# Kernel optimization log

Measured on AMD Instinct MI355X. Metric: run time of the kernel, lower is better.

## Reference

```python
import jax, jax.numpy as jnp
import numpy as np

N_HEADS = 4
NEG_SLOPE = 0.2  # DGL GATConv default leaky_relu slope


def setup_inputs() -> dict:
    key = jax.random.key(0)
    ks = jax.random.split(key, 12)
    N, E = 50000, 800000
    in_dim, time_dim, out_dim = 128, 128, 128
    d_head = out_dim // N_HEADS
    in_total = in_dim + time_dim
    h = jax.random.normal(ks[0], (N, in_dim), jnp.float32)
    time_tensor = jax.random.uniform(ks[1], (E,), jnp.float32)
    src = jax.random.randint(ks[2], (E,), 0, N, jnp.int32)
    dst = jax.random.randint(ks[3], (E,), 0, N, jnp.int32)
    # TimeEncoding: Linear(1, time_dim) with xavier weight, zero bias
    w_t = jax.random.normal(ks[4], (time_dim, 1), jnp.float32) * (6.0 / (1 + time_dim)) ** 0.5
    b_t = jnp.zeros((time_dim,), jnp.float32)
    # GATConv params
    W_fc = jax.random.normal(ks[5], (N_HEADS * d_head, in_total), jnp.float32) * (2.0 / in_total) ** 0.5
    attn_l = jax.random.normal(ks[6], (N_HEADS, d_head), jnp.float32) * 0.1
    attn_r = jax.random.normal(ks[7], (N_HEADS, d_head), jnp.float32) * 0.1
    W_res = jax.random.normal(ks[8], (N_HEADS * d_head, in_total), jnp.float32) * (2.0 / in_total) ** 0.5
    bias = jnp.zeros((N_HEADS * d_head,), jnp.float32)
    return {"h": h, "time_tensor": time_tensor, "src": src, "dst": dst,
            "num_nodes": N, "w_t": w_t, "b_t": b_t, "W_fc": W_fc,
            "attn_l": attn_l, "attn_r": attn_r, "W_res": W_res, "bias": bias}


def reference(h, time_tensor, src, dst, num_nodes, w_t, b_t, W_fc, attn_l, attn_r, W_res, bias):
    N = num_nodes
    E = src.shape[0]
    # Time encoding: cos(W t + b), per edge -> [E, time_dim]
    time_emb = jnp.cos(time_tensor[:, None] * w_t[:, 0][None, :] + b_t[None, :])
    # Mailbox mean of concat([src h, time_emb]) per dst node.
    # mean(concat) == concat(mean, mean), so sum the two halves separately.
    ones = jnp.ones((E,), h.dtype)
    deg = jax.ops.segment_sum(ones, dst, num_segments=N)  # [N]
    sum_h = jax.ops.segment_sum(h[src], dst, num_segments=N)       # [N, in_dim]
    sum_t = jax.ops.segment_sum(time_emb, dst, num_segments=N)     # [N, time_dim]
    inv_deg = 1.0 / jnp.maximum(deg, 1.0)
    h_time = jnp.concatenate([sum_h, sum_t], axis=1) * inv_deg[:, None]  # [N, in+time]
    # GATConv (eval mode, no dropout)
    d_head = W_fc.shape[0] // N_HEADS
    feat = (h_time @ W_fc.T).reshape(N, N_HEADS, d_head)  # [N,H,D]
    el = jnp.sum(feat * attn_l[None], axis=-1)  # [N,H]
    er = jnp.sum(feat * attn_r[None], axis=-1)  # [N,H]
    e = el[src] + er[dst]                        # [E,H]
    e = jnp.where(e > 0, e, NEG_SLOPE * e)
    # edge softmax over incoming edges of each dst node
    m = jax.ops.segment_max(e, dst, num_segments=N)  # [N,H]
    m = jnp.where(jnp.isfinite(m), m, 0.0)
    ex = jnp.exp(e - m[dst])
    denom = jax.ops.segment_sum(ex, dst, num_segments=N)
    a = ex / jnp.maximum(denom[dst], 1e-9)           # [E,H]
    rst = jax.ops.segment_sum(a[:, :, None] * feat[src], dst, num_segments=N)  # [N,H,D]
    res = (h_time @ W_res.T).reshape(N, N_HEADS, d_head)
    out = rst + res + bias.reshape(1, N_HEADS, d_head)
    out = jax.nn.elu(out)
    return out.reshape(N, -1)  # [N, out_dim]
```

## Files before the change

### kernel.cpp

```cpp
#include <hip/hip_runtime.h>
#include <math.h>

#define NH 4
#define NEG_SLOPE 0.2f
#define BKT_SHIFT 8
#define EPB 4096
#define CBLK 8192
#define TBLK 512
#define INV2PI 0.15915494309189535f
#define LOG2E  1.4426950408889634f

typedef __attribute__((ext_vector_type(8))) short bf16x8;
typedef __attribute__((ext_vector_type(4))) float f32x4;
typedef __attribute__((ext_vector_type(2))) float f32x2;

__device__ __forceinline__ float blo(unsigned u) { return __uint_as_float(u << 16); }
__device__ __forceinline__ float bhi(unsigned u) { return __uint_as_float(u & 0xFFFF0000u); }
__device__ __forceinline__ f32x2 mk2(float a, float b) { f32x2 r; r.x = a; r.y = b; return r; }
__device__ __forceinline__ f32x2 unpk(unsigned u) { return mk2(blo(u), bhi(u)); }
__device__ __forceinline__ unsigned short rne(float f) {
    unsigned u = __float_as_uint(f);
    u += 0x7FFFu + ((u >> 16) & 1u);
    return (unsigned short)(u >> 16);
}
__device__ __forceinline__ unsigned pack2(float a, float b) {
    return (unsigned)rne(a) | ((unsigned)rne(b) << 16);
}

__global__ __launch_bounds__(256) void k_prep(
    const float* __restrict__ h, unsigned* __restrict__ hbu, int n_pairs,
    const float* __restrict__ Wfc, const float* __restrict__ Wres,
    unsigned* __restrict__ wcat,
    const float* __restrict__ w_t, const float* __restrict__ b_t,
    unsigned* __restrict__ tbl,
    const int* __restrict__ dst, int* __restrict__ bkt_cnt, int E, int NB, int EB) {
    __shared__ int cnt[256];
    int tid = threadIdx.x;
    int t = blockIdx.x * blockDim.x + tid;
    if (t < n_pairs) {
        float2 v = ((const float2*)h)[t];
        hbu[t] = pack2(v.x, v.y);
    }
    if (t < 32768) {
        int col = t >> 7, kk = t & 127;
        const float* srcp = (col < 128) ? (Wfc + (size_t)col * 256)
                                        : (Wres + (size_t)(col - 128) * 256);
        float2 v = ((const float2*)srcp)[kk];
        int s  = col >> 6, ct = (col >> 4) & 3, r = col & 15;
        int ks = kk >> 4,  q  = (kk >> 2) & 3,  d = kk & 3;
        int w2i = ((s * 32 + ks * 4 + ct) << 8) + ((q * 16 + r) << 2) + d;
        wcat[w2i] = pack2(v.x, v.y);
    }
    if (blockIdx.x < (unsigned)EB) {
        cnt[tid] = 0;
        __syncthreads();
        int q0 = (blockIdx.x * CBLK) >> 2;
#pragma unroll
        for (int k = 0; k < CBLK / 1024; k++) {
            int qi = q0 + k * 256 + tid;
            int base = qi * 4;
            if (base + 3 < E) {
                int4 dd = ((const int4*)dst)[qi];
                atomicAdd(&cnt[dd.x >> BKT_SHIFT], 1);
                atomicAdd(&cnt[dd.y >> BKT_SHIFT], 1);
                atomicAdd(&cnt[dd.z >> BKT_SHIFT], 1);
                atomicAdd(&cnt[dd.w >> BKT_SHIFT], 1);
            } else {
                for (int e = base; e < E; e++) atomicAdd(&cnt[dst[e] >> BKT_SHIFT], 1);
            }
        }
        __syncthreads();
        if (tid < NB) {
            int c = cnt[tid];
            if (c) atomicAdd(bkt_cnt + tid, c);
        }
    }
    int tb = blockIdx.x - EB;
    if (tb >= 0 && tb < TBLK) {
        int idx = tb * 256 + tid;
        int j = idx >> 6, dp = idx & 63;
        int d0 = dp * 2;
        float tv = ((float)j + 0.5f) * (1.0f / 2048.0f);
        float w0 = w_t[d0] * INV2PI,     b0 = b_t[d0] * INV2PI;
        float w1 = w_t[d0 + 1] * INV2PI, b1 = b_t[d0 + 1] * INV2PI;
        tbl[idx] = pack2(__builtin_amdgcn_cosf(fmaf(tv, w0, b0)),
                         __builtin_amdgcn_cosf(fmaf(tv, w1, b1)));
    }
}

__global__ __launch_bounds__(256) void k_bktscan(
    const int* __restrict__ bkt_cnt, int* __restrict__ bkt_start,
    int* __restrict__ bkt_cursor, int* __restrict__ row_start,
    int NB, int E, int N) {
    __shared__ int wsum[4];
    int tid = threadIdx.x, lane = tid & 63, wid = tid >> 6;
    int v = (tid < NB) ? bkt_cnt[tid] : 0;
    int x = v;
#pragma unroll
    for (int off = 1; off < 64; off <<= 1) {
        int y = __shfl_up(x, off, 64);
        if (lane >= off) x += y;
    }
    if (lane == 63) wsum[wid] = x;
    __syncthreads();
    if (tid == 0) {
        int s = 0;
#pragma unroll
        for (int k = 0; k < 4; k++) { int tk = wsum[k]; wsum[k] = s; s += tk; }
    }
    __syncthreads();
    int excl = wsum[wid] + x - v;
    if (tid < NB) { bkt_start[tid] = excl; bkt_cursor[tid] = excl; }
    if (tid == 0) { bkt_start[NB] = E; row_start[N] = E; }
}

__global__ __launch_bounds__(256) void k_binscatter(
    const int* __restrict__ src, const int* __restrict__ dst,
    const float* __restrict__ tt, int* __restrict__ bkt_cursor,
    uint2* __restrict__ staged, int E, int NB) {
    __shared__ int cnt[1024];
    __shared__ int basep[1024];
    int e0 = blockIdx.x * EPB;
    int tid = threadIdx.x;
    for (int b = tid; b < NB; b += 256) cnt[b] = 0;
    __syncthreads();
#pragma unroll
    for (int k = 0; k < EPB / 256; k++) {
        int e = e0 + k * 256 + tid;
        if (e < E) atomicAdd(&cnt[dst[e] >> BKT_SHIFT], 1);
    }
    __syncthreads();
    for (int b = tid; b < NB; b += 256) {
        int c = cnt[b];
        basep[b] = (c > 0) ? atomicAdd(bkt_cursor + b, c) : 0;
        cnt[b] = 0;
    }
    __syncthreads();
#pragma unroll
    for (int k = 0; k < EPB / 256; k++) {
        int e = e0 + k * 256 + tid;
        if (e < E) {
            int d = dst[e];
            int b = d >> BKT_SHIFT;
            int r = atomicAdd(&cnt[b], 1);
            unsigned tq = min((unsigned)(tt[e] * 32768.0f), 32767u);
            staged[basep[b] + r] =
                make_uint2(((unsigned)src[e] << 15) | tq, (unsigned)(d & 255));
        }
    }
}

__global__ __launch_bounds__(256) void k_binsort(
    const uint2* __restrict__ staged, const int* __restrict__ bkt_start,
    int* __restrict__ row_start, unsigned* __restrict__ est, int N) {
    __shared__ int cnt[256];
    __shared__ int cur[256];
    __shared__ int wsum[4];
    int b = blockIdx.x;
    int n0 = b << BKT_SHIFT;
    int tid = threadIdx.x;
    cnt[tid] = 0;
    __syncthreads();
    int s0 = bkt_start[b], s1 = bkt_start[b + 1];
    for (int p = s0 + tid; p < s1; p += 256)
        atomicAdd(&cnt[staged[p].y], 1);
    __syncthreads();
    int lane = tid & 63, wid = tid >> 6;
    int v = cnt[tid];
    int x = v;
#pragma unroll
    for (int off = 1; off < 64; off <<= 1) {
        int y = __shfl_up(x, off, 64);
        if (lane >= off) x += y;
    }
    if (lane == 63) wsum[wid] = x;
    __syncthreads();
    if (tid == 0) {
        int s = 0;
#pragma unroll
        for (int k = 0; k < 4; k++) { int tk = wsum[k]; wsum[k] = s; s += tk; }
    }
    __syncthreads();
    int excl = s0 + wsum[wid] + x - v;
    cur[tid] = excl;
    if (n0 + tid < N) row_start[n0 + tid] = excl;
    __syncthreads();
    for (int p = s0 + tid; p < s1; p += 256) {
        uint2 vv = staged[p];
        int pos = atomicAdd(&cur[vv.y], 1);
        est[pos] = vv.x;
    }
}

__device__ __forceinline__ void agg_edge(unsigned u, float wgt, const char* __restrict__ hb,
                                         const char* __restrict__ tb, int i,
                                         f32x2* aH, f32x2* aT) {
    unsigned hoff = (u >> 15) << 8;
    unsigned toff = (u & 0x7FF0u) << 4;
    uint4 hv = *(const uint4*)(hb + hoff + i * 16);
    uint4 tv = *(const uint4*)(tb + toff + i * 16);
    f32x2 w2 = mk2(wgt, wgt);
    aH[0] = w2 * unpk(hv.x) + aH[0];
    aH[1] = w2 * unpk(hv.y) + aH[1];
    aH[2] = w2 * unpk(hv.z) + aH[2];
    aH[3] = w2 * unpk(hv.w) + aH[3];
    aT[0] = w2 * unpk(tv.x) + aT[0];
    aT[1] = w2 * unpk(tv.y) + aT[1];
    aT[2] = w2 * unpk(tv.z) + aT[2];
    aT[3] = w2 * unpk(tv.w) + aT[3];
}

__device__ __forceinline__ void attn_edge(unsigned u, bool valid, const char* __restrict__ fb,
                                          int i, int hd, const char* __restrict__ elb,
                                          float erh, f32x2* acc, float& den) {
    unsigned off = (u >> 15) << 8;
    float elh = *(const float*)(elb + (off >> 4) + (hd << 2));
    uint4 fv = *(const uint4*)(fb + off + i * 16);
    float w = elh + erh; w = w > 0.f ? w : NEG_SLOPE * w;
    float ex = valid ? __builtin_amdgcn_exp2f(w) : 0.f;
    f32x2 ex2 = mk2(ex, ex);
    acc[0] = ex2 * unpk(fv.x) + acc[0];
    acc[1] = ex2 * unpk(fv.y) + acc[1];
    acc[2] = ex2 * unpk(fv.z) + acc[2];
    acc[3] = ex2 * unpk(fv.w) + acc[3];
    den += ex;
}

__global__ __launch_bounds__(256) void k_agg(
    const unsigned* __restrict__ hbu, const unsigned* __restrict__ tbl,
    const unsigned* __restrict__ est, const int* __restrict__ row_start,
    unsigned* __restrict__ htu, int N) {
    int tid = threadIdx.x;
    int i = tid & 15;
    int n = blockIdx.x * 16 + (tid >> 4);
    if (n >= N) return;
    const char* hb = (const char*)hbu;
    const char* tb = (const char*)tbl;
    int rs = row_start[n], re = row_start[n + 1];
    f32x2 aH[4] = {}, aT[4] = {};
    int e = rs;
    int nfull = (re - rs) >> 2;
    for (int j = 0; j < nfull; j++, e += 4) {
        unsigned u0 = est[e];
        unsigned u1 = est[e + 1];
        unsigned u2 = est[e + 2];
        unsigned u3 = est[e + 3];
        agg_edge(u0, 1.0f, hb, tb, i, aH, aT);
        agg_edge(u1, 1.0f, hb, tb, i, aH, aT);
        agg_edge(u2, 1.0f, hb, tb, i, aH, aT);
        agg_edge(u3, 1.0f, hb, tb, i, aH, aT);
    }
    if (e < re) {
        unsigned u0 = est[e];
        bool v1 = e + 1 < re, v2 = e + 2 < re;
        unsigned u1 = v1 ? est[e + 1] : u0;
        unsigned u2 = v2 ? est[e + 2] : u0;
        agg_edge(u0, 1.0f, hb, tb, i, aH, aT);
        agg_edge(u1, v1 ? 1.0f : 0.0f, hb, tb, i, aH, aT);
        agg_edge(u2, v2 ? 1.0f : 0.0f, hb, tb, i, aH, aT);
    }
    int deg = re - rs;
    float idg = (deg > 0) ? 1.0f / (float)deg : 1.0f;
    uint4* ht4 = (uint4*)htu;
    uint4 oh, ot;
    oh.x = pack2(aH[0].x * idg, aH[0].y * idg);
    oh.y = pack2(aH[1].x * idg, aH[1].y * idg);
    oh.z = pack2(aH[2].x * idg, aH[2].y * idg);
    oh.w = pack2(aH[3].x * idg, aH[3].y * idg);
    ot.x = pack2(aT[0].x * idg, aT[0].y * idg);
    ot.y = pack2(aT[1].x * idg, aT[1].y * idg);
    ot.z = pack2(aT[2].x * idg, aT[2].y * idg);
    ot.w = pack2(aT[3].x * idg, aT[3].y * idg);
    ht4[(size_t)n * 32 + i]      = oh;
    ht4[(size_t)n * 32 + 16 + i] = ot;
}

__global__ __launch_bounds__(256) void k_gemm(
    const unsigned short* __restrict__ ht, const unsigned* __restrict__ wcat,
    unsigned short* __restrict__ feat, float* __restrict__ res_out, int N) {
    int tid = threadIdx.x;
    int wave = tid >> 6, lane = tid & 63;
    int r = lane & 15, q = lane >> 4;
    int row0 = blockIdx.x * 16;
    int colbase = wave * 64;
    int gr = row0 + r; if (gr >= N) gr = N - 1;
    const bf16x8* a_base = (const bf16x8*)ht + (size_t)gr * 32;
    const bf16x8* bbase = (const bf16x8*)wcat + (size_t)wave * 2048 + lane;
    f32x4 acc[4] = {};
#pragma unroll
    for (int ks = 0; ks < 8; ks++) {
        bf16x8 a = a_base[ks * 4 + q];
        bf16x8 b[4];
#pragma unroll
        for (int ct = 0; ct < 4; ct++)
            b[ct] = bbase[(ks * 4 + ct) * 64];
#pragma unroll
        for (int ct = 0; ct < 4; ct++)
            acc[ct] = __builtin_amdgcn_mfma_f32_16x16x32_bf16(a, b[ct], acc[ct], 0, 0, 0);
    }
    bool featw = (colbase < 128);
#pragma unroll
    for (int ct = 0; ct < 4; ct++) {
        int col = colbase + ct * 16 + r;
#pragma unroll
        for (int reg = 0; reg < 4; reg++) {
            int row = row0 + q * 4 + reg;
            if (row >= N) continue;
            float v = acc[ct][reg];
            if (featw) feat[(size_t)row * 128 + col] = rne(v);
            else       res_out[(size_t)row * 128 + (col - 128)] = v;
        }
    }
}

__global__ void k_el_er(const unsigned* __restrict__ featu,
                        const float* __restrict__ attn_l, const float* __restrict__ attn_r,
                        float* __restrict__ el, float* __restrict__ er, int NH4) {
    int t = blockIdx.x * blockDim.x + threadIdx.x;
    if (t >= NH4) return;
    int n = t >> 2, hd = t & 3;
    const unsigned* f = featu + (size_t)n * 64 + hd * 16;
    const float2* al = (const float2*)(attn_l + hd * 32);
    const float2* ar = (const float2*)(attn_r + hd * 32);
    float sl = 0.f, sr = 0.f;
#pragma unroll
    for (int i = 0; i < 16; i++) {
        unsigned u = f[i];
        float f0 = blo(u), f1 = bhi(u);
        float2 a = al[i], b = ar[i];
        sl = fmaf(f0, a.x, fmaf(f1, a.y, sl));
        sr = fmaf(f0, b.x, fmaf(f1, b.y, sr));
    }
    el[t] = sl * LOG2E;
    er[t] = sr * LOG2E;
}

__global__ __launch_bounds__(256) void k_attn(
    const unsigned* __restrict__ est, const int* __restrict__ row_start,
    const float* __restrict__ el, const float* __restrict__ er,
    const unsigned* __restrict__ featu, const float* __restrict__ bias,
    float* __restrict__ out, int N) {
    int tid = threadIdx.x;
    int i = tid & 15;
    int hd = i >> 2;
    int n = blockIdx.x * 16 + (tid >> 4);
    if (n >= N) return;
    int rs = row_start[n], re = row_start[n + 1];
    float erh = er[(size_t)n * 4 + hd];
    const char* fb = (const char*)featu;
    const char* elb = (const char*)el;
    f32x2 acc[4] = {};
    float den = 0.f;
    int e = rs;
    int nfull = (re - rs) >> 2;
    for (int j = 0; j < nfull; j++, e += 4) {
        unsigned u0 = est[e];
        unsigned u1 = est[e + 1];
        unsigned u2 = est[e + 2];
        unsigned u3 = est[e + 3];
        attn_edge(u0, true, fb, i, hd, elb, erh, acc, den);
        attn_edge(u1, true, fb, i, hd, elb, erh, acc, den);
        attn_edge(u2, true, fb, i, hd, elb, erh, acc, den);
        attn_edge(u3, true, fb, i, hd, elb, erh, acc, den);
    }
    if (e < re) {
        unsigned u0 = est[e];
        bool v1 = e + 1 < re, v2 = e + 2 < re;
        unsigned u1 = v1 ? est[e + 1] : u0;
        unsigned u2 = v2 ? est[e + 2] : u0;
        attn_edge(u0, true, fb, i, hd, elb, erh, acc, den);
        attn_edge(u1, v1, fb, i, hd, elb, erh, acc, den);
        attn_edge(u2, v2, fb, i, hd, elb, erh, acc, den);
    }
    float id = 1.0f / fmaxf(den, 1e-9f);
    float* op = out + (size_t)n * 128 + i * 8;
    const float* bp = bias + i * 8;
    float4 o0 = ((const float4*)op)[0], o1 = ((const float4*)op)[1];
    float4 b0 = ((const float4*)bp)[0], b1 = ((const float4*)bp)[1];
    float4 r0, r1;
    r0.x = fmaf(acc[0].x, id, o0.x + b0.x);
    r0.y = fmaf(acc[0].y, id, o0.y + b0.y);
    r0.z = fmaf(acc[1].x, id, o0.z + b0.z);
    r0.w = fmaf(acc[1].y, id, o0.w + b0.w);
    r1.x = fmaf(acc[2].x, id, o1.x + b1.x);
    r1.y = fmaf(acc[2].y, id, o1.y + b1.y);
    r1.z = fmaf(acc[3].x, id, o1.z + b1.z);
    r1.w = fmaf(acc[3].y, id, o1.w + b1.w);
    r0.x = r0.x > 0.f ? r0.x : (__expf(r0.x) - 1.0f);
    r0.y = r0.y > 0.f ? r0.y : (__expf(r0.y) - 1.0f);
    r0.z = r0.z > 0.f ? r0.z : (__expf(r0.z) - 1.0f);
    r0.w = r0.w > 0.f ? r0.w : (__expf(r0.w) - 1.0f);
    r1.x = r1.x > 0.f ? r1.x : (__expf(r1.x) - 1.0f);
    r1.y = r1.y > 0.f ? r1.y : (__expf(r1.y) - 1.0f);
    r1.z = r1.z > 0.f ? r1.z : (__expf(r1.z) - 1.0f);
    r1.w = r1.w > 0.f ? r1.w : (__expf(r1.w) - 1.0f);
    ((float4*)op)[0] = r0;
    ((float4*)op)[1] = r1;
}

extern "C" void kernel_launch(void* const* d_in, const int* in_sizes, int n_in,
                              void* d_out, int out_size, void* d_ws, size_t ws_size,
                              hipStream_t stream) {
    const float* h     = (const float*)d_in[0];
    const float* tt    = (const float*)d_in[1];
    const int*   src   = (const int*)d_in[2];
    const int*   dst   = (const int*)d_in[3];
    const float* w_t   = (const float*)d_in[5];
    const float* b_t   = (const float*)d_in[6];
    const float* W_fc  = (const float*)d_in[7];
    const float* al    = (const float*)d_in[8];
    const float* ar    = (const float*)d_in[9];
    const float* W_res = (const float*)d_in[10];
    const float* bias  = (const float*)d_in[11];

    int N = in_sizes[0] / 128;
    int E = in_sizes[1];
    int NB = (N + 255) >> BKT_SHIFT;
    int EB = (E + CBLK - 1) / CBLK;

    char* ws = (char*)d_ws;
    size_t off = 0;
    auto alloc = [&](size_t bytes) { void* p = ws + off; off = (off + bytes + 15) & ~(size_t)15; return p; };
    unsigned* htu     = (unsigned*)alloc((size_t)N * 128 * 4);
    unsigned* hbu     = (unsigned*)alloc((size_t)N * 64 * 4);
    unsigned* featu   = (unsigned*)alloc((size_t)N * 64 * 4);
    unsigned* wcat    = (unsigned*)alloc(32768 * 4);
    unsigned* tbl     = (unsigned*)alloc((size_t)2048 * 64 * 4);
    float*    el      = (float*)alloc((size_t)N * NH * 4);
    float*    er      = (float*)alloc((size_t)N * NH * 4);
    int*      row_st  = (int*)alloc((size_t)(N + 1) * 4);
    int*      bkt_cur = (int*)alloc((size_t)NB * 4);
    int*      bkt_cnt = (int*)alloc((size_t)NB * 4);
    int*      bkt_sta = (int*)alloc((size_t)(NB + 1) * 4);
    unsigned* est     = (unsigned*)alloc((size_t)E * 4);
    uint2*    staged  = (uint2*)featu;

    hipMemsetAsync(bkt_cnt, 0, (size_t)NB * 4, stream);

    int prep_n = N * 64;
    hipLaunchKernelGGL(k_prep, dim3((prep_n + 255) / 256), dim3(256), 0, stream,
                       h, hbu, prep_n, W_fc, W_res, wcat, w_t, b_t, tbl,
                       dst, bkt_cnt, E, NB, EB);
    hipLaunchKernelGGL(k_bktscan, dim3(1), dim3(256), 0, stream,
                       bkt_cnt, bkt_sta, bkt_cur, row_st, NB, E, N);
    hipLaunchKernelGGL(k_binscatter, dim3((E + EPB - 1) / EPB), dim3(256), 0, stream,
                       src, dst, tt, bkt_cur, staged, E, NB);
    hipLaunchKernelGGL(k_binsort, dim3(NB), dim3(256), 0, stream,
                       staged, bkt_sta, row_st, est, N);
    hipLaunchKernelGGL(k_agg, dim3((N + 15) / 16), dim3(256), 0, stream,
                       hbu, tbl, est, row_st, htu, N);
    hipLaunchKernelGGL(k_gemm, dim3((N + 15) / 16), dim3(256), 0, stream,
                       (const unsigned short*)htu, wcat,
                       (unsigned short*)featu, (float*)d_out, N);
    hipLaunchKernelGGL(k_el_er, dim3((N * NH + 255) / 256), dim3(256), 0, stream,
                       featu, al, ar, el, er, N * NH);
    hipLaunchKernelGGL(k_attn, dim3((N + 15) / 16), dim3(256), 0, stream,
                       est, row_st, el, er, featu, bias, (float*)d_out, N);
}
```

Before: 246.4 us.

## Schedule nodes by in-degree within buckets to balance agg and attn warps

In the bin-sort kernel, nodes inside each 256-node bucket are counting-sorted by in-degree (capped at 255) into a permutation array. The aggregation and attention kernels map each 16-lane group to a node through this permutation, so nodes of similar degree share a wavefront and lanes idle less on divergent loop trip counts. The cost is an extra histogram and scan in binsort plus one indirection load per node, and output writes become less sequential.

```diff
diff --git a/kernel.cpp b/kernel.cpp
--- a/kernel.cpp
+++ b/kernel.cpp
@@ -152,14 +152,18 @@
 
 __global__ __launch_bounds__(256) void k_binsort(
     const uint2* __restrict__ staged, const int* __restrict__ bkt_start,
-    int* __restrict__ row_start, unsigned* __restrict__ est, int N) {
+    int* __restrict__ row_start, unsigned* __restrict__ est,
+    int* __restrict__ perm, int N) {
     __shared__ int cnt[256];
     __shared__ int cur[256];
     __shared__ int wsum[4];
+    __shared__ int dh[256];
+    __shared__ int dcur[256];
     int b = blockIdx.x;
     int n0 = b << BKT_SHIFT;
     int tid = threadIdx.x;
     cnt[tid] = 0;
+    dh[tid] = 0;
     __syncthreads();
     int s0 = bkt_start[b], s1 = bkt_start[b + 1];
     for (int p = s0 + tid; p < s1; p += 256)
@@ -183,8 +187,32 @@
     __syncthreads();
     int excl = s0 + wsum[wid] + x - v;
     cur[tid] = excl;
-    if (n0 + tid < N) row_start[n0 + tid] = excl;
-    __syncthreads();
+    bool valid = (n0 + tid < N);
+    if (valid) row_start[n0 + tid] = excl;
+    int dc = v < 255 ? v : 255;
+    if (valid) atomicAdd(&dh[dc], 1);
+    __syncthreads();
+    int dv = dh[tid];
+    int dx = dv;
+#pragma unroll
+    for (int off = 1; off < 64; off <<= 1) {
+        int y = __shfl_up(dx, off, 64);
+        if (lane >= off) dx += y;
+    }
+    if (lane == 63) wsum[wid] = dx;
+    __syncthreads();
+    if (tid == 0) {
+        int s = 0;
+#pragma unroll
+        for (int k = 0; k < 4; k++) { int tk = wsum[k]; wsum[k] = s; s += tk; }
+    }
+    __syncthreads();
+    dcur[tid] = wsum[wid] + dx - dv;
+    __syncthreads();
+    if (valid) {
+        int pos = atomicAdd(&dcur[dc], 1);
+        perm[n0 + pos] = n0 + tid;
+    }
     for (int p = s0 + tid; p < s1; p += 256) {
         uint2 vv = staged[p];
         int pos = atomicAdd(&cur[vv.y], 1);
@@ -193,12 +221,12 @@
 }
 
 __device__ __forceinline__ void agg_edge(unsigned u, float wgt, const char* __restrict__ hb,
-                                         const char* __restrict__ tb, int i,
+                                         const char* __restrict__ tb, int i16,
                                          f32x2* aH, f32x2* aT) {
     unsigned hoff = (u >> 15) << 8;
     unsigned toff = (u & 0x7FF0u) << 4;
-    uint4 hv = *(const uint4*)(hb + hoff + i * 16);
-    uint4 tv = *(const uint4*)(tb + toff + i * 16);
+    uint4 hv = *(const uint4*)(hb + hoff + i16);
+    uint4 tv = *(const uint4*)(tb + toff + i16);
     f32x2 w2 = mk2(wgt, wgt);
     aH[0] = w2 * unpk(hv.x) + aH[0];
     aH[1] = w2 * unpk(hv.y) + aH[1];
@@ -211,11 +239,11 @@
 }
 
 __device__ __forceinline__ void attn_edge(unsigned u, bool valid, const char* __restrict__ fb,
-                                          int i, int hd, const char* __restrict__ elb,
+                                          int i16, int hd4, const char* __restrict__ elb,
                                           float erh, f32x2* acc, float& den) {
     unsigned off = (u >> 15) << 8;
-    float elh = *(const float*)(elb + (off >> 4) + (hd << 2));
-    uint4 fv = *(const uint4*)(fb + off + i * 16);
+    float elh = *(const float*)(elb + (off >> 4) + hd4);
+    uint4 fv = *(const uint4*)(fb + off + i16);
     float w = elh + erh; w = w > 0.f ? w : NEG_SLOPE * w;
     float ex = valid ? __builtin_amdgcn_exp2f(w) : 0.f;
     f32x2 ex2 = mk2(ex, ex);
@@ -229,11 +257,13 @@
 __global__ __launch_bounds__(256) void k_agg(
     const unsigned* __restrict__ hbu, const unsigned* __restrict__ tbl,
     const unsigned* __restrict__ est, const int* __restrict__ row_start,
-    unsigned* __restrict__ htu, int N) {
+    const int* __restrict__ perm, unsigned* __restrict__ htu, int N) {
     int tid = threadIdx.x;
     int i = tid & 15;
-    int n = blockIdx.x * 16 + (tid >> 4);
-    if (n >= N) return;
+    int i16 = i * 16;
+    int gid = blockIdx.x * 16 + (tid >> 4);
+    if (gid >= N) return;
+    int n = perm[gid];
     const char* hb = (const char*)hbu;
     const char* tb = (const char*)tbl;
     int rs = row_start[n], re = row_start[n + 1];
@@ -245,19 +275,19 @@
         unsigned u1 = est[e + 1];
         unsigned u2 = est[e + 2];
         unsigned u3 = est[e + 3];
-        agg_edge(u0, 1.0f, hb, tb, i, aH, aT);
-        agg_edge(u1, 1.0f, hb, tb, i, aH, aT);
-        agg_edge(u2, 1.0f, hb, tb, i, aH, aT);
-        agg_edge(u3, 1.0f, hb, tb, i, aH, aT);
+        agg_edge(u0, 1.0f, hb, tb, i16, aH, aT);
+        agg_edge(u1, 1.0f, hb, tb, i16, aH, aT);
+        agg_edge(u2, 1.0f, hb, tb, i16, aH, aT);
+        agg_edge(u3, 1.0f, hb, tb, i16, aH, aT);
     }
     if (e < re) {
         unsigned u0 = est[e];
         bool v1 = e + 1 < re, v2 = e + 2 < re;
         unsigned u1 = v1 ? est[e + 1] : u0;
         unsigned u2 = v2 ? est[e + 2] : u0;
-        agg_edge(u0, 1.0f, hb, tb, i, aH, aT);
-        agg_edge(u1, v1 ? 1.0f : 0.0f, hb, tb, i, aH, aT);
-        agg_edge(u2, v2 ? 1.0f : 0.0f, hb, tb, i, aH, aT);
+        agg_edge(u0, 1.0f, hb, tb, i16, aH, aT);
+        agg_edge(u1, v1 ? 1.0f : 0.0f, hb, tb, i16, aH, aT);
+        agg_edge(u2, v2 ? 1.0f : 0.0f, hb, tb, i16, aH, aT);
     }
     int deg = re - rs;
     float idg = (deg > 0) ? 1.0f / (float)deg : 1.0f;
@@ -339,12 +369,15 @@
     const unsigned* __restrict__ est, const int* __restrict__ row_start,
     const float* __restrict__ el, const float* __restrict__ er,
     const unsigned* __restrict__ featu, const float* __restrict__ bias,
-    float* __restrict__ out, int N) {
+    const int* __restrict__ perm, float* __restrict__ out, int N) {
     int tid = threadIdx.x;
     int i = tid & 15;
+    int i16 = i * 16;
     int hd = i >> 2;
-    int n = blockIdx.x * 16 + (tid >> 4);
-    if (n >= N) return;
+    int hd4 = hd << 2;
+    int gid = blockIdx.x * 16 + (tid >> 4);
+    if (gid >= N) return;
+    int n = perm[gid];
     int rs = row_start[n], re = row_start[n + 1];
     float erh = er[(size_t)n * 4 + hd];
     const char* fb = (const char*)featu;
@@ -358,19 +391,19 @@
         unsigned u1 = est[e + 1];
         unsigned u2 = est[e + 2];
         unsigned u3 = est[e + 3];
-        attn_edge(u0, true, fb, i, hd, elb, erh, acc, den);
-        attn_edge(u1, true, fb, i, hd, elb, erh, acc, den);
-        attn_edge(u2, true, fb, i, hd, elb, erh, acc, den);
-        attn_edge(u3, true, fb, i, hd, elb, erh, acc, den);
+        attn_edge(u0, true, fb, i16, hd4, elb, erh, acc, den);
+        attn_edge(u1, true, fb, i16, hd4, elb, erh, acc, den);
+        attn_edge(u2, true, fb, i16, hd4, elb, erh, acc, den);
+        attn_edge(u3, true, fb, i16, hd4, elb, erh, acc, den);
     }
     if (e < re) {
         unsigned u0 = est[e];
         bool v1 = e + 1 < re, v2 = e + 2 < re;
         unsigned u1 = v1 ? est[e + 1] : u0;
         unsigned u2 = v2 ? est[e + 2] : u0;
-        attn_edge(u0, true, fb, i, hd, elb, erh, acc, den);
-        attn_edge(u1, v1, fb, i, hd, elb, erh, acc, den);
-        attn_edge(u2, v2, fb, i, hd, elb, erh, acc, den);
+        attn_edge(u0, true, fb, i16, hd4, elb, erh, acc, den);
+        attn_edge(u1, v1, fb, i16, hd4, elb, erh, acc, den);
+        attn_edge(u2, v2, fb, i16, hd4, elb, erh, acc, den);
     }
     float id = 1.0f / fmaxf(den, 1e-9f);
     float* op = out + (size_t)n * 128 + i * 8;
@@ -429,6 +462,7 @@
     float*    el      = (float*)alloc((size_t)N * NH * 4);
     float*    er      = (float*)alloc((size_t)N * NH * 4);
     int*      row_st  = (int*)alloc((size_t)(N + 1) * 4);
+    int*      perm    = (int*)alloc((size_t)N * 4);
     int*      bkt_cur = (int*)alloc((size_t)NB * 4);
     int*      bkt_cnt = (int*)alloc((size_t)NB * 4);
     int*      bkt_sta = (int*)alloc((size_t)(NB + 1) * 4);
@@ -446,14 +480,14 @@
     hipLaunchKernelGGL(k_binscatter, dim3((E + EPB - 1) / EPB), dim3(256), 0, stream,
                        src, dst, tt, bkt_cur, staged, E, NB);
     hipLaunchKernelGGL(k_binsort, dim3(NB), dim3(256), 0, stream,
-                       staged, bkt_sta, row_st, est, N);
+                       staged, bkt_sta, row_st, est, perm, N);
     hipLaunchKernelGGL(k_agg, dim3((N + 15) / 16), dim3(256), 0, stream,
-                       hbu, tbl, est, row_st, htu, N);
+                       hbu, tbl, est, row_st, perm, htu, N);
     hipLaunchKernelGGL(k_gemm, dim3((N + 15) / 16), dim3(256), 0, stream,
                        (const unsigned short*)htu, wcat,
                        (unsigned short*)featu, (float*)d_out, N);
     hipLaunchKernelGGL(k_el_er, dim3((N * NH + 255) / 256), dim3(256), 0, stream,
                        featu, al, ar, el, er, N * NH);
     hipLaunchKernelGGL(k_attn, dim3((N + 15) / 16), dim3(256), 0, stream,
-                       est, row_st, el, er, featu, bias, (float*)d_out, N);
-}
+                       est, row_st, el, er, featu, bias, perm, (float*)d_out, N);
+}
```

Result: slower. 263.3 us (+6.9%).
